# Performance work log

Hardware: AMD Instinct MI355X
Metric: run time of the kernel (lower is better)

## Reference

```python
import jax, jax.numpy as jnp
import numpy as np

B, T, P, D, H = 4, 12, 196, 512, 8
DH = D // H
EPS = 1e-6


def _norm(x, alpha, bias):
    # torch Norm: alpha*(x-mean)/(std_unbiased+eps)+bias, std uses Bessel correction (ddof=1)
    mu = jnp.mean(x, axis=-1, keepdims=True)
    sd = jnp.std(x, axis=-1, ddof=1, keepdims=True)
    return alpha * (x - mu) / (sd + EPS) + bias


def setup_inputs() -> dict:
    key = jax.random.key(0)
    ks = jax.random.split(key, 12)
    s = 0.02

    def n(k, shape, scale=s):
        return jax.random.normal(k, shape, jnp.float32) * scale

    return {
        "x": jax.random.normal(ks[0], (B, T, P, D), jnp.float32),
        "Wq": n(ks[1], (D, D)), "bq": jnp.zeros((D,), jnp.float32),
        "Wk": n(ks[2], (D, D)), "bk": jnp.zeros((D,), jnp.float32),
        "Wv": n(ks[3], (D, D)), "bv": jnp.zeros((D,), jnp.float32),
        "in_a": jnp.ones((D,), jnp.float32), "in_b": jnp.zeros((D,), jnp.float32),
        "attn_a": jnp.ones((D,), jnp.float32), "attn_b": jnp.zeros((D,), jnp.float32),
        "out_a": jnp.ones((D,), jnp.float32), "out_b": jnp.zeros((D,), jnp.float32),
        "Wt": n(ks[4], (T, D, D)), "bt": jnp.zeros((T, D), jnp.float32),
        "pos": n(ks[5], (T, T, P, D), 0.02),
        "W1": n(ks[6], (2 * D, D)), "b1": jnp.zeros((2 * D,), jnp.float32),
        "W2": n(ks[7], (D, 2 * D)), "b2": jnp.zeros((D,), jnp.float32),
    }


def reference(x, Wq, bq, Wk, bk, Wv, bv, in_a, in_b, attn_a, attn_b,
              out_a, out_b, Wt, bt, pos, W1, b1, W2, b2):
    x2 = _norm(x, in_a, in_b)

    def proj(W, b):
        # [B,T,P,D] -> [B,T,H,P,DH]
        return (x2 @ W.T + b).reshape(B, T, P, H, DH).transpose(0, 1, 3, 2, 4)

    Q = proj(Wq, bq)
    K = proj(Wk, bk)
    V = proj(Wv, bv)

    # all-pairs temporal cross attention: [B,t,u,H,Pq,Pk]
    qk = jnp.einsum('btijk,builk->btuijl', Q, K) / np.sqrt(DH)
    attn = jax.nn.softmax(qk, axis=-1)  # no mask, dropout=0
    av = jnp.einsum('btuijl,builk->btuijk', attn, V)  # [B,t,u,H,P,DH]
    av = av.transpose(0, 1, 2, 4, 3, 5).reshape(B, T, T, P, D)
    av = _norm(av, attn_a, attn_b)
    x2p = av + pos  # pos broadcasts over batch

    # per-u Linear fused as one batched contraction, summed over u
    tc = jnp.einsum('btupd,ued->btpe', x2p / T, Wt) + jnp.sum(bt, axis=0)
    x = x + jax.nn.gelu(tc, approximate=False)

    x2 = _norm(x, out_a, out_b)
    h = jax.nn.gelu(x2 @ W1.T + b1, approximate=False)
    y = jax.nn.gelu(h @ W2.T + b2, approximate=False)
    return x + y
```

## Files before the change

kernel.cpp:

```cpp
#include <hip/hip_runtime.h>
#include <hip/hip_bf16.h>

typedef __hip_bfloat16 bf16;

typedef __bf16 bfrag8 __attribute__((ext_vector_type(8)));
typedef __bf16 bfrag4 __attribute__((ext_vector_type(4)));
typedef float  ffrag4 __attribute__((ext_vector_type(4)));
typedef float  ffrag16 __attribute__((ext_vector_type(16)));

#define EPS 1e-6f

__device__ __forceinline__ float gelu_exact(float v) {
  return 0.5f * v * (1.0f + erff(v * 0.7071067811865475f));
}

__device__ __forceinline__ void async16(const void* g, void* s) {
  __builtin_amdgcn_global_load_lds(
      (const __attribute__((address_space(1))) unsigned int*)g,
      (__attribute__((address_space(3))) unsigned int*)s, 16, 0, 0);
}

struct alignas(16) bf16x8 { bf16 v[8]; };
struct alignas(4)  bf16p2 { __bf16 v[2]; };

__global__ __launch_bounds__(256) void zero_acc_kernel(float* __restrict__ p) {
  size_t i = ((size_t)blockIdx.x * 256 + threadIdx.x) * 4;
  *(float4*)(p + i) = make_float4(0.f, 0.f, 0.f, 0.f);
}

__global__ __launch_bounds__(256) void conv_w_kernel(
    const float* __restrict__ Wq, const float* __restrict__ Wk,
    const float* __restrict__ Wv, const float* __restrict__ W1,
    const float* __restrict__ W2, const float* __restrict__ Wt,
    __bf16* __restrict__ dst)
{
  size_t e = ((size_t)blockIdx.x * 256 + threadIdx.x) * 8;
  const float* src; size_t off, dsto;
  if      (e <  262144) { src = Wq; off = e;           dsto = e; }
  else if (e <  524288) { src = Wk; off = e -  262144; dsto = e; }
  else if (e <  786432) { src = Wv; off = e -  524288; dsto = e; }
  else if (e < 1310720) { src = W1; off = e -  786432; dsto = e; }
  else if (e < 1835008) { src = W2; off = e - 1310720; dsto = e; }
  else if (e < 4980736) {
    src = Wt; off = e - 1835008;
    size_t u = off >> 18;
    size_t rem = off & 262143;
    size_t eo = rem >> 9, d = rem & 511;
    dsto = 1835008 + eo * 6144 + u * 512 + d;
  }
  else return;
  float4 f0 = *(const float4*)(src + off);
  float4 f1 = *(const float4*)(src + off + 4);
  bfrag8 o;
  o[0] = (__bf16)f0.x; o[1] = (__bf16)f0.y; o[2] = (__bf16)f0.z; o[3] = (__bf16)f0.w;
  o[4] = (__bf16)f1.x; o[5] = (__bf16)f1.y; o[6] = (__bf16)f1.z; o[7] = (__bf16)f1.w;
  *(bfrag8*)(dst + dsto) = o;
}

__global__ __launch_bounds__(512) void sum_bt_kernel(
    const float* __restrict__ bt, float* __restrict__ sbt)
{
  int n = threadIdx.x;
  float s = 0.f;
#pragma unroll
  for (int u = 0; u < 12; ++u) s += bt[u * 512 + n];
  sbt[n] = s;
}

__global__ __launch_bounds__(64) void norm_f32_to_bf16_kernel(
    const float* __restrict__ in, __bf16* __restrict__ out,
    const float* __restrict__ alpha, const float* __restrict__ beta)
{
  size_t row = blockIdx.x;
  int l = threadIdx.x;
  const float* r = in + row * 512 + l * 8;
  float4 v0 = *(const float4*)(r);
  float4 v1 = *(const float4*)(r + 4);
  float f[8] = {v0.x, v0.y, v0.z, v0.w, v1.x, v1.y, v1.z, v1.w};
  float s = 0.f, ss = 0.f;
#pragma unroll
  for (int q = 0; q < 8; ++q) { s += f[q]; ss += f[q] * f[q]; }
#pragma unroll
  for (int off = 32; off; off >>= 1) { s += __shfl_xor(s, off); ss += __shfl_xor(ss, off); }
  float mu = s * (1.f / 512.f);
  float var = fmaxf((ss - 512.f * mu * mu) * (1.f / 511.f), 0.f);
  float inv = 1.f / (sqrtf(var) + EPS);
  const float* al = alpha + l * 8;
  const float* be = beta + l * 8;
  float4 a0 = *(const float4*)al, a1 = *(const float4*)(al + 4);
  float4 b0 = *(const float4*)be, b1 = *(const float4*)(be + 4);
  float aa[8] = {a0.x, a0.y, a0.z, a0.w, a1.x, a1.y, a1.z, a1.w};
  float bb[8] = {b0.x, b0.y, b0.z, b0.w, b1.x, b1.y, b1.z, b1.w};
  bfrag8 o;
#pragma unroll
  for (int q = 0; q < 8; ++q) o[q] = (__bf16)(aa[q] * (f[q] - mu) * inv + bb[q]);
  *(bfrag8*)(out + row * 512 + l * 8) = o;
}

__global__ __launch_bounds__(256) void norm_av_kernel(
    bf16* __restrict__ av, const float* __restrict__ alpha,
    const float* __restrict__ beta, const float* __restrict__ pos)
{
  size_t row = (size_t)blockIdx.x * 4 + (threadIdx.x >> 6);
  int l = threadIdx.x & 63;
  bf16* r = av + row * 512 + (size_t)l * 8;
  bf16x8 ib = *(const bf16x8*)r;
  float f[8];
#pragma unroll
  for (int q = 0; q < 8; ++q) f[q] = __bfloat162float(ib.v[q]);
  float s = 0.f, ss = 0.f;
#pragma unroll
  for (int q = 0; q < 8; ++q) { s += f[q]; ss += f[q] * f[q]; }
#pragma unroll
  for (int off = 32; off; off >>= 1) { s += __shfl_xor(s, off); ss += __shfl_xor(ss, off); }
  float mu = s * (1.f / 512.f);
  float var = fmaxf((ss - 512.f * mu * mu) * (1.f / 511.f), 0.f);
  float inv = 1.f / (sqrtf(var) + EPS);
  size_t prow = row % 28224;
  const float* pr = pos + prow * 512 + l * 8;
  float4 p0 = *(const float4*)pr, p1 = *(const float4*)(pr + 4);
  const float* al = alpha + l * 8;
  const float* be = beta + l * 8;
  float4 a0 = *(const float4*)al, a1 = *(const float4*)(al + 4);
  float4 b0 = *(const float4*)be, b1 = *(const float4*)(be + 4);
  float pa[8] = {p0.x, p0.y, p0.z, p0.w, p1.x, p1.y, p1.z, p1.w};
  float aa[8] = {a0.x, a0.y, a0.z, a0.w, a1.x, a1.y, a1.z, a1.w};
  float bb[8] = {b0.x, b0.y, b0.z, b0.w, b1.x, b1.y, b1.z, b1.w};
  bf16x8 ob;
#pragma unroll
  for (int q = 0; q < 8; ++q)
    ob.v[q] = __float2bfloat16(aa[q] * (f[q] - mu) * inv + bb[q] + pa[q]);
  *(bf16x8*)r = ob;
}

__global__ __launch_bounds__(256) void mfma_nt_kernel(
    const __bf16* __restrict__ A,
    const __bf16* __restrict__ Bq, const __bf16* __restrict__ Bk,
    const __bf16* __restrict__ Bv,
    const float* __restrict__ bq, const float* __restrict__ bk,
    const float* __restrict__ bv,
    __bf16* __restrict__ oq, __bf16* __restrict__ ok, __bf16* __restrict__ ov,
    const float* __restrict__ res, float* __restrict__ fout,
    int K, int mode)
{
  __shared__ __bf16 As[2 * 128 * 32];
  __shared__ __bf16 Bs[2 * 128 * 32];
  int tid = threadIdx.x;

  int nwg = gridDim.x * gridDim.y;
  int cpx = nwg >> 3;
  int lid = blockIdx.x + gridDim.x * blockIdx.y;
  int logical = (lid & 7) * cpx + (lid >> 3);
  int bx = logical % gridDim.x;
  int by = logical / gridDim.x;
  int m0 = by * 128;
  int n0g = bx * 128;

  const __bf16* Bsel; const float* biassel; __bf16* osel; int ncol0;
  if (mode == 0) {
    int sel = n0g >> 9;
    Bsel = sel == 0 ? Bq : (sel == 1 ? Bk : Bv);
    biassel = sel == 0 ? bq : (sel == 1 ? bk : bv);
    osel = sel == 0 ? oq : (sel == 1 ? ok : ov);
    ncol0 = n0g & 511;
  } else {
    Bsel = Bq; biassel = bq; osel = oq; ncol0 = n0g;
  }

  int srow = tid >> 2;
  int scol = ((tid & 3) ^ ((srow >> 1) & 3)) * 8;
  int rg0 = m0 + srow;       if (rg0 > 9407) rg0 = 9407;
  int rg1 = m0 + 64 + srow;  if (rg1 > 9407) rg1 = 9407;
  const __bf16* a0 = A + (size_t)rg0 * K + scol;
  const __bf16* a1 = A + (size_t)rg1 * K + scol;
  const __bf16* b0 = Bsel + (size_t)(ncol0 + srow) * K + scol;
  const __bf16* b1 = Bsel + (size_t)(ncol0 + 64 + srow) * K + scol;
  char* sa0 = (char*)As + tid * 16;
  char* sa1 = (char*)As + 4096 + tid * 16;
  char* sb0 = (char*)Bs + tid * 16;
  char* sb1 = (char*)Bs + 4096 + tid * 16;

  int l = tid & 63, w = tid >> 6;
  int lm = l & 15, lq = l >> 4;
  int wm = w >> 1, wn = w & 1;
  int rsw = ((((lm >> 1) & 3) ^ lq)) * 8;

  const int nsteps = K >> 5;
  async16(a0, sa0);
  async16(a1, sa1);
  async16(b0, sb0);
  async16(b1, sb1);
  __syncthreads();

  ffrag4 acc[4][4] = {};
  int cur = 0;
  for (int t = 0; t < nsteps; ++t) {
    if (t + 1 < nsteps) {
      int k1 = (t + 1) << 5;
      int bo = (cur ^ 1) * 8192;
      async16(a0 + k1, sa0 + bo);
      async16(a1 + k1, sa1 + bo);
      async16(b0 + k1, sb0 + bo);
      async16(b1 + k1, sb1 + bo);
    }
    int co = cur * 4096;
    bfrag8 af[4], bfr[4];
#pragma unroll
    for (int i = 0; i < 4; ++i)
      af[i] = *(const bfrag8*)&As[co + (wm * 64 + i * 16 + lm) * 32 + rsw];
#pragma unroll
    for (int j = 0; j < 4; ++j)
      bfr[j] = *(const bfrag8*)&Bs[co + (wn * 64 + j * 16 + lm) * 32 + rsw];
#pragma unroll
    for (int i = 0; i < 4; ++i)
#pragma unroll
      for (int j = 0; j < 4; ++j)
        acc[i][j] = __builtin_amdgcn_mfma_f32_16x16x32_bf16(af[i], bfr[j], acc[i][j], 0, 0, 0);
    __syncthreads();
    cur ^= 1;
  }

#pragma unroll
  for (int i = 0; i < 4; ++i) {
    int mbase = m0 + wm * 64 + i * 16 + lq * 4;
#pragma unroll
    for (int j = 0; j < 4; ++j) {
      int n = ncol0 + wn * 64 + j * 16 + lm;
      float bj = biassel[n];
#pragma unroll
      for (int r = 0; r < 4; ++r) {
        int mr = mbase + r;
        if (mr < 9408) {
          float v = acc[i][j][r] + bj;
          if (mode == 0)      osel[(size_t)mr * 512 + n] = (__bf16)v;
          else if (mode == 1) osel[(size_t)mr * 1024 + n] = (__bf16)gelu_exact(v);
          else                fout[(size_t)mr * 512 + n] =
                                res[(size_t)mr * 512 + n] + gelu_exact(v);
        }
      }
    }
  }
}

__global__ __launch_bounds__(256) void mfma_tc_kernel(
    const __bf16* __restrict__ X2p, const __bf16* __restrict__ Wte,
    float* __restrict__ accb)
{
  __shared__ __bf16 As[2 * 128 * 32];
  __shared__ __bf16 Bs[2 * 128 * 32];
  int tid = threadIdx.x;

  int lid = blockIdx.x + 4 * (blockIdx.y + 74 * blockIdx.z);
  int logical = (lid & 7) * 148 + (lid >> 3);
  int lx = logical & 3;
  int rest = logical >> 2;
  int ly = rest % 74;
  int lz = rest / 74;

  int m0 = ly * 128;
  int n0 = lx * 128;
  int kbeg = lz * 1536;

  int srow = tid >> 2;
  int scol = ((tid & 3) ^ ((srow >> 1) & 3)) * 8;
  int rg0 = m0 + srow;       if (rg0 > 9407) rg0 = 9407;
  int rg1 = m0 + 64 + srow;  if (rg1 > 9407) rg1 = 9407;
  int btq0 = rg0 / 196, p0_ = rg0 - btq0 * 196;
  int btq1 = rg1 / 196, p1_ = rg1 - btq1 * 196;
  const __bf16* a0 = X2p + (size_t)btq0 * 1204224 + (size_t)p0_ * 512 + scol;
  const __bf16* a1 = X2p + (size_t)btq1 * 1204224 + (size_t)p1_ * 512 + scol;
  const __bf16* b0 = Wte + (size_t)(n0 + srow) * 6144 + scol;
  const __bf16* b1 = Wte + (size_t)(n0 + 64 + srow) * 6144 + scol;
  char* sa0 = (char*)As + tid * 16;
  char* sa1 = (char*)As + 4096 + tid * 16;
  char* sb0 = (char*)Bs + tid * 16;
  char* sb1 = (char*)Bs + 4096 + tid * 16;

  int l = tid & 63, w = tid >> 6;
  int lm = l & 15, lq = l >> 4;
  int wm = w >> 1, wn = w & 1;
  int rsw = ((((lm >> 1) & 3) ^ lq)) * 8;

  {
    size_t aoff = (size_t)(kbeg >> 9) * 100352 + (size_t)(kbeg & 511);
    async16(a0 + aoff, sa0);
    async16(a1 + aoff, sa1);
    async16(b0 + kbeg, sb0);
    async16(b1 + kbeg, sb1);
  }
  __syncthreads();

  ffrag4 acc[4][4] = {};
  int cur = 0;
  for (int t = 0; t < 48; ++t) {
    if (t + 1 < 48) {
      int k1 = kbeg + (t + 1) * 32;
      size_t aoff = (size_t)(k1 >> 9) * 100352 + (size_t)(k1 & 511);
      int bo = (cur ^ 1) * 8192;
      async16(a0 + aoff, sa0 + bo);
      async16(a1 + aoff, sa1 + bo);
      async16(b0 + k1, sb0 + bo);
      async16(b1 + k1, sb1 + bo);
    }
    int co = cur * 4096;
    bfrag8 af[4], bfr[4];
#pragma unroll
    for (int i = 0; i < 4; ++i)
      af[i] = *(const bfrag8*)&As[co + (wm * 64 + i * 16 + lm) * 32 + rsw];
#pragma unroll
    for (int j = 0; j < 4; ++j)
      bfr[j] = *(const bfrag8*)&Bs[co + (wn * 64 + j * 16 + lm) * 32 + rsw];
#pragma unroll
    for (int i = 0; i < 4; ++i)
#pragma unroll
      for (int j = 0; j < 4; ++j)
        acc[i][j] = __builtin_amdgcn_mfma_f32_16x16x32_bf16(af[i], bfr[j], acc[i][j], 0, 0, 0);
    __syncthreads();
    cur ^= 1;
  }

#pragma unroll
  for (int i = 0; i < 4; ++i) {
    int mbase = m0 + wm * 64 + i * 16 + lq * 4;
#pragma unroll
    for (int j = 0; j < 4; ++j) {
      int n = n0 + wn * 64 + j * 16 + lm;
#pragma unroll
      for (int r = 0; r < 4; ++r) {
        int mr = mbase + r;
        if (mr < 9408)
          atomicAdd(accb + (size_t)mr * 512 + n, acc[i][j][r]);
      }
    }
  }
}

__global__ __launch_bounds__(64) void tc_epi_norm_kernel(
    const float* __restrict__ accb, const float* __restrict__ x,
    const float* __restrict__ sbt,
    const float* __restrict__ alpha, const float* __restrict__ beta,
    float* __restrict__ xmid, __bf16* __restrict__ x3b)
{
  size_t row = blockIdx.x;
  int l = threadIdx.x;
  size_t base = row * 512 + l * 8;
  float4 c0 = *(const float4*)(accb + base);
  float4 c1 = *(const float4*)(accb + base + 4);
  float4 x0 = *(const float4*)(x + base);
  float4 x1 = *(const float4*)(x + base + 4);
  float4 s0 = *(const float4*)(sbt + l * 8);
  float4 s1 = *(const float4*)(sbt + l * 8 + 4);
  float cc[8] = {c0.x, c0.y, c0.z, c0.w, c1.x, c1.y, c1.z, c1.w};
  float xx[8] = {x0.x, x0.y, x0.z, x0.w, x1.x, x1.y, x1.z, x1.w};
  float sv[8] = {s0.x, s0.y, s0.z, s0.w, s1.x, s1.y, s1.z, s1.w};
  float f[8];
#pragma unroll
  for (int q = 0; q < 8; ++q)
    f[q] = xx[q] + gelu_exact(cc[q] * (1.f / 12.f) + sv[q]);
  *(float4*)(xmid + base)     = make_float4(f[0], f[1], f[2], f[3]);
  *(float4*)(xmid + base + 4) = make_float4(f[4], f[5], f[6], f[7]);
  float s = 0.f, ss = 0.f;
#pragma unroll
  for (int q = 0; q < 8; ++q) { s += f[q]; ss += f[q] * f[q]; }
#pragma unroll
  for (int off = 32; off; off >>= 1) { s += __shfl_xor(s, off); ss += __shfl_xor(ss, off); }
  float mu = s * (1.f / 512.f);
  float var = fmaxf((ss - 512.f * mu * mu) * (1.f / 511.f), 0.f);
  float inv = 1.f / (sqrtf(var) + EPS);
  const float* al = alpha + l * 8;
  const float* be = beta + l * 8;
  float4 a0 = *(const float4*)al, a1 = *(const float4*)(al + 4);
  float4 b0 = *(const float4*)be, b1 = *(const float4*)(be + 4);
  float aa[8] = {a0.x, a0.y, a0.z, a0.w, a1.x, a1.y, a1.z, a1.w};
  float bb[8] = {b0.x, b0.y, b0.z, b0.w, b1.x, b1.y, b1.z, b1.w};
  bfrag8 o;
#pragma unroll
  for (int q = 0; q < 8; ++q) o[q] = (__bf16)(aa[q] * (f[q] - mu) * inv + bb[q]);
  *(bfrag8*)(x3b + base) = o;
}

__global__ __launch_bounds__(512, 4) void attn_kernel(
    const __bf16* __restrict__ Q, const __bf16* __restrict__ K,
    const __bf16* __restrict__ V, __bf16* __restrict__ av)
{
  __shared__ __bf16 Ks[196 * 64];
  __shared__ __bf16 Vt[64 * 208];
  __shared__ __bf16 Pball[8 * 32 * 20];

  int bid = blockIdx.x;
  int half = bid & 1;
  int h = (bid >> 1) & 7;
  int r0 = bid >> 4;
  int u = r0 % 12;
  int b = r0 / 12;

  const __bf16* Kp = K + ((size_t)(b * 12 + u) * 196) * 512 + h * 64;
  const __bf16* Vp = V + ((size_t)(b * 12 + u) * 196) * 512 + h * 64;

  for (int idx = threadIdx.x; idx < 196 * 8; idx += 512) {
    int r = idx >> 3, g = idx & 7;
    *(bfrag8*)&Ks[r * 64 + ((g ^ (r & 7)) * 8)] =
        *(const bfrag8*)&Kp[(size_t)r * 512 + g * 8];
  }
  for (int idx = threadIdx.x; idx < 64 * 6; idx += 512) {
    int r = idx / 6, c2 = 196 + (idx % 6) * 2;
    bf16p2 z; z.v[0] = (__bf16)0.f; z.v[1] = (__bf16)0.f;
    *(bf16p2*)&Vt[r * 208 + c2] = z;
  }
  for (int idx = threadIdx.x; idx < 98 * 8; idx += 512) {
    int r2 = (idx % 98) * 2, c8 = (idx / 98) * 8;
    bfrag8 va = *(const bfrag8*)&Vp[(size_t)r2 * 512 + c8];
    bfrag8 vb = *(const bfrag8*)&Vp[(size_t)(r2 + 1) * 512 + c8];
#pragma unroll
    for (int e = 0; e < 8; ++e) {
      bf16p2 pr; pr.v[0] = va[e]; pr.v[1] = vb[e];
      *(bf16p2*)&Vt[(c8 + e) * 208 + r2] = pr;
    }
  }
  __syncthreads();

  int w = threadIdx.x >> 6, l = threadIdx.x & 63;
  int l5 = l >> 5, c = l & 31;
  __bf16* Pb = Pball + w * (32 * 20);

  for (int unit = w; unit < 42; unit += 8) {
    int t = unit / 7, qt = unit - t * 7;
    int tq = half * 6 + t;
    const __bf16* Qp = Q + ((size_t)(b * 12 + tq) * 196) * 512 + h * 64;
    __bf16* avp = av + ((size_t)((b * 12 + tq) * 12 + u) * 196) * 512 + h * 64;
    int q0 = qt * 32;

    const __bf16* qp = Qp + (size_t)(q0 + c) * 512 + l5 * 8;
    bfrag8 qf[4];
    qf[0] = *(const bfrag8*)(qp);
    qf[1] = *(const bfrag8*)(qp + 16);
    qf[2] = *(const bfrag8*)(qp + 32);
    qf[3] = *(const bfrag8*)(qp + 48);

    ffrag16 O0, O1;
#pragma unroll
    for (int g = 0; g < 16; ++g) { O0[g] = 0.f; O1[g] = 0.f; }
    float sumacc = 0.f;

    for (int nt = 0; nt < 7; ++nt) {
      int key = nt * 32 + c; if (key > 195) key = 195;
      const __bf16* kbase = &Ks[key * 64];
      int kx = key & 7;

      ffrag16 s;
#pragma unroll
      for (int g = 0; g < 16; ++g) s[g] = 0.f;
#pragma unroll
      for (int kc = 0; kc < 4; ++kc) {
        bfrag8 kf = *(const bfrag8*)&kbase[(((kc * 2 + l5) ^ kx) * 8)];
        s = __builtin_amdgcn_mfma_f32_32x32x16_bf16(kf, qf[kc], s, 0, 0, 0);
      }

#pragma unroll
      for (int g = 0; g < 16; ++g) {
        float e = __expf(s[g] * 0.125f);
        bool keep = (nt < 6) || ((g < 4) && (l5 == 0));
        e = keep ? e : 0.f;
        s[g] = e;
        sumacc += e;
      }

#pragma unroll
      for (int sub = 0; sub < 2; ++sub) {
        if (nt == 6 && sub == 1) break;
#pragma unroll
        for (int g = 0; g < 8; ++g) {
          int gg = sub * 8 + g;
          int k16 = (gg & 3) + 8 * ((gg >> 2) & 1) + 4 * l5;
          Pb[c * 20 + k16] = (__bf16)s[gg];
        }
        __threadfence_block();
        int ch = nt * 2 + sub;
        bfrag4 plo = *(const bfrag4*)&Pb[c * 20 + l5 * 8];
        bfrag4 phi = *(const bfrag4*)&Pb[c * 20 + l5 * 8 + 4];
        bfrag8 pa = __builtin_shufflevector(plo, phi, 0, 1, 2, 3, 4, 5, 6, 7);
        bfrag8 v0 = *(const bfrag8*)&Vt[(size_t)(c     ) * 208 + ch * 16 + l5 * 8];
        bfrag8 v1 = *(const bfrag8*)&Vt[(size_t)(c + 32) * 208 + ch * 16 + l5 * 8];
        O0 = __builtin_amdgcn_mfma_f32_32x32x16_bf16(pa, v0, O0, 0, 0, 0);
        O1 = __builtin_amdgcn_mfma_f32_32x32x16_bf16(pa, v1, O1, 0, 0, 0);
      }
    }

    float stot = sumacc + __shfl_xor(sumacc, 32);

#pragma unroll
    for (int g = 0; g < 16; ++g) {
      int row = (g & 3) + 8 * (g >> 2) + 4 * l5;
      float sq = __shfl(stot, row);
      float iv = __builtin_amdgcn_rcpf(sq);
      int q = q0 + row;
      if (q < 196) {
        size_t base = (size_t)q * 512 + c;
        avp[base]      = (__bf16)(O0[g] * iv);
        avp[base + 32] = (__bf16)(O1[g] * iv);
      }
    }
  }
}

extern "C" void kernel_launch(void* const* d_in, const int* in_sizes, int n_in,
                              void* d_out, int out_size, void* d_ws, size_t ws_size,
                              hipStream_t stream)
{
  const float* x      = (const float*)d_in[0];
  const float* Wq     = (const float*)d_in[1];
  const float* bq     = (const float*)d_in[2];
  const float* Wk     = (const float*)d_in[3];
  const float* bk     = (const float*)d_in[4];
  const float* Wv     = (const float*)d_in[5];
  const float* bv     = (const float*)d_in[6];
  const float* in_a   = (const float*)d_in[7];
  const float* in_b   = (const float*)d_in[8];
  const float* attn_a = (const float*)d_in[9];
  const float* attn_b = (const float*)d_in[10];
  const float* out_a  = (const float*)d_in[11];
  const float* out_b  = (const float*)d_in[12];
  const float* Wt     = (const float*)d_in[13];
  const float* bt     = (const float*)d_in[14];
  const float* pos    = (const float*)d_in[15];
  const float* W1     = (const float*)d_in[16];
  const float* b1     = (const float*)d_in[17];
  const float* W2     = (const float*)d_in[18];
  const float* b2     = (const float*)d_in[19];

  char* ws = (char*)d_ws;
  const size_t bfb = (size_t)9408 * 512 * 2;
  __bf16* x2b  = (__bf16*)(ws);
  __bf16* Qb   = (__bf16*)(ws + bfb);
  __bf16* Kb   = (__bf16*)(ws + 2 * bfb);
  __bf16* Vb   = (__bf16*)(ws + 3 * bfb);
  __bf16* av   = (__bf16*)(ws + 4 * bfb);
  char*   wreg = ws + 4 * bfb + (size_t)115605504;
  __bf16* Wqb  = (__bf16*)(wreg);
  __bf16* Wkb  = (__bf16*)(wreg) + 262144;
  __bf16* Wvb  = (__bf16*)(wreg) + 524288;
  __bf16* W1b  = (__bf16*)(wreg) + 786432;
  __bf16* W2b  = (__bf16*)(wreg) + 1310720;
  __bf16* Wtb  = (__bf16*)(wreg) + 1835008;
  float*  sbt  = (float*)(wreg + 9961472);
  float*  accb = (float*)(wreg + 9963520);
  float*  xmid = (float*)(ws);
  __bf16* x3b  = (__bf16*)(ws + 2 * bfb);
  __bf16* hb   = (__bf16*)(ws + 4 * bfb);
  float*  out  = (float*)d_out;

  conv_w_kernel<<<2432, 256, 0, stream>>>(Wq, Wk, Wv, W1, W2, Wt, (__bf16*)wreg);
  sum_bt_kernel<<<1, 512, 0, stream>>>(bt, sbt);
  zero_acc_kernel<<<4704, 256, 0, stream>>>(accb);
  norm_f32_to_bf16_kernel<<<9408, 64, 0, stream>>>(x, x2b, in_a, in_b);
  mfma_nt_kernel<<<dim3(12, 74), 256, 0, stream>>>(
      x2b, Wqb, Wkb, Wvb, bq, bk, bv, Qb, Kb, Vb, nullptr, nullptr, 512, 0);
  attn_kernel<<<768, 512, 0, stream>>>(Qb, Kb, Vb, av);
  norm_av_kernel<<<28224, 256, 0, stream>>>((bf16*)av, attn_a, attn_b, pos);
  mfma_tc_kernel<<<dim3(4, 74, 4), 256, 0, stream>>>(av, Wtb, accb);
  tc_epi_norm_kernel<<<9408, 64, 0, stream>>>(accb, x, sbt, out_a, out_b, xmid, x3b);
  mfma_nt_kernel<<<dim3(8, 74), 256, 0, stream>>>(
      x3b, W1b, nullptr, nullptr, b1, nullptr, nullptr, hb, nullptr, nullptr,
      nullptr, nullptr, 512, 1);
  mfma_nt_kernel<<<dim3(4, 74), 256, 0, stream>>>(
      hb, W2b, nullptr, nullptr, b2, nullptr, nullptr, nullptr, nullptr, nullptr,
      xmid, out, 1024, 2);
}
```

Measured before the change: 544.7 us.

## Triple-buffer LDS tiles with two-deep async prefetch in MFMA GEMM kernels

Both MFMA GEMM kernels move from double- to triple-buffered shared memory tiles and prefetch two K-steps ahead. The full __syncthreads is replaced by a partial s_waitcnt vmcnt(4) plus a raw s_barrier, so one stage of global-to-LDS loads can stay in flight across the barrier. The goal is to hide global load latency behind MFMA work. In exchange, LDS per block grows from 32KB to 48KB, which may lower occupancy, and correctness now depends on manual vmcnt accounting matching the compiler's emitted loads.

```diff
diff --git a/kernel.cpp b/kernel.cpp
--- a/kernel.cpp
+++ b/kernel.cpp
@@ -143,8 +143,8 @@
     const float* __restrict__ res, float* __restrict__ fout,
     int K, int mode)
 {
-  __shared__ __bf16 As[2 * 128 * 32];
-  __shared__ __bf16 Bs[2 * 128 * 32];
+  __shared__ __bf16 As[3 * 128 * 32];
+  __shared__ __bf16 Bs[3 * 128 * 32];
   int tid = threadIdx.x;
 
   int nwg = gridDim.x * gridDim.y;
@@ -186,22 +186,24 @@
   int rsw = ((((lm >> 1) & 3) ^ lq)) * 8;
 
   const int nsteps = K >> 5;
-  async16(a0, sa0);
-  async16(a1, sa1);
-  async16(b0, sb0);
-  async16(b1, sb1);
-  __syncthreads();
+  async16(a0, sa0); async16(a1, sa1);
+  async16(b0, sb0); async16(b1, sb1);
+  async16(a0 + 32, sa0 + 8192); async16(a1 + 32, sa1 + 8192);
+  async16(b0 + 32, sb0 + 8192); async16(b1 + 32, sb1 + 8192);
+  __builtin_amdgcn_sched_barrier(0);
+  asm volatile("s_waitcnt vmcnt(4)" ::: "memory");
+  __builtin_amdgcn_s_barrier();
+  __builtin_amdgcn_sched_barrier(0);
 
   ffrag4 acc[4][4] = {};
   int cur = 0;
   for (int t = 0; t < nsteps; ++t) {
-    if (t + 1 < nsteps) {
-      int k1 = (t + 1) << 5;
-      int bo = (cur ^ 1) * 8192;
-      async16(a0 + k1, sa0 + bo);
-      async16(a1 + k1, sa1 + bo);
-      async16(b0 + k1, sb0 + bo);
-      async16(b1 + k1, sb1 + bo);
+    if (t + 2 < nsteps) {
+      int k2 = (t + 2) << 5;
+      int nb = cur + 2; if (nb >= 3) nb -= 3;
+      int bo = nb * 8192;
+      async16(a0 + k2, sa0 + bo); async16(a1 + k2, sa1 + bo);
+      async16(b0 + k2, sb0 + bo); async16(b1 + k2, sb1 + bo);
     }
     int co = cur * 4096;
     bfrag8 af[4], bfr[4];
@@ -216,8 +218,12 @@
 #pragma unroll
       for (int j = 0; j < 4; ++j)
         acc[i][j] = __builtin_amdgcn_mfma_f32_16x16x32_bf16(af[i], bfr[j], acc[i][j], 0, 0, 0);
-    __syncthreads();
-    cur ^= 1;
+    __builtin_amdgcn_sched_barrier(0);
+    if (t + 2 < nsteps) asm volatile("s_waitcnt vmcnt(4)" ::: "memory");
+    else                asm volatile("s_waitcnt vmcnt(0)" ::: "memory");
+    __builtin_amdgcn_s_barrier();
+    __builtin_amdgcn_sched_barrier(0);
+    cur += 1; if (cur == 3) cur = 0;
   }
 
 #pragma unroll
@@ -246,8 +252,8 @@
     const __bf16* __restrict__ X2p, const __bf16* __restrict__ Wte,
     float* __restrict__ accb)
 {
-  __shared__ __bf16 As[2 * 128 * 32];
-  __shared__ __bf16 Bs[2 * 128 * 32];
+  __shared__ __bf16 As[3 * 128 * 32];
+  __shared__ __bf16 Bs[3 * 128 * 32];
   int tid = threadIdx.x;
 
   int lid = blockIdx.x + 4 * (blockIdx.y + 74 * blockIdx.z);
@@ -282,25 +288,29 @@
   int rsw = ((((lm >> 1) & 3) ^ lq)) * 8;
 
   {
-    size_t aoff = (size_t)(kbeg >> 9) * 100352 + (size_t)(kbeg & 511);
-    async16(a0 + aoff, sa0);
-    async16(a1 + aoff, sa1);
-    async16(b0 + kbeg, sb0);
-    async16(b1 + kbeg, sb1);
-  }
-  __syncthreads();
+    size_t ao0 = (size_t)(kbeg >> 9) * 100352 + (size_t)(kbeg & 511);
+    int k1 = kbeg + 32;
+    size_t ao1 = (size_t)(k1 >> 9) * 100352 + (size_t)(k1 & 511);
+    async16(a0 + ao0, sa0); async16(a1 + ao0, sa1);
+    async16(b0 + kbeg, sb0); async16(b1 + kbeg, sb1);
+    async16(a0 + ao1, sa0 + 8192); async16(a1 + ao1, sa1 + 8192);
+    async16(b0 + k1, sb0 + 8192); async16(b1 + k1, sb1 + 8192);
+  }
+  __builtin_amdgcn_sched_barrier(0);
+  asm volatile("s_waitcnt vmcnt(4)" ::: "memory");
+  __builtin_amdgcn_s_barrier();
+  __builtin_amdgcn_sched_barrier(0);
 
   ffrag4 acc[4][4] = {};
   int cur = 0;
   for (int t = 0; t < 48; ++t) {
-    if (t + 1 < 48) {
-      int k1 = kbeg + (t + 1) * 32;
-      size_t aoff = (size_t)(k1 >> 9) * 100352 + (size_t)(k1 & 511);
-      int bo = (cur ^ 1) * 8192;
-      async16(a0 + aoff, sa0 + bo);
-      async16(a1 + aoff, sa1 + bo);
-      async16(b0 + k1, sb0 + bo);
-      async16(b1 + k1, sb1 + bo);
+    if (t + 2 < 48) {
+      int k2 = kbeg + (t + 2) * 32;
+      size_t aoff = (size_t)(k2 >> 9) * 100352 + (size_t)(k2 & 511);
+      int nb = cur + 2; if (nb >= 3) nb -= 3;
+      int bo = nb * 8192;
+      async16(a0 + aoff, sa0 + bo); async16(a1 + aoff, sa1 + bo);
+      async16(b0 + k2, sb0 + bo); async16(b1 + k2, sb1 + bo);
     }
     int co = cur * 4096;
     bfrag8 af[4], bfr[4];
@@ -315,8 +325,12 @@
 #pragma unroll
       for (int j = 0; j < 4; ++j)
         acc[i][j] = __builtin_amdgcn_mfma_f32_16x16x32_bf16(af[i], bfr[j], acc[i][j], 0, 0, 0);
-    __syncthreads();
-    cur ^= 1;
+    __builtin_amdgcn_sched_barrier(0);
+    if (t + 2 < 48) asm volatile("s_waitcnt vmcnt(4)" ::: "memory");
+    else            asm volatile("s_waitcnt vmcnt(0)" ::: "memory");
+    __builtin_amdgcn_s_barrier();
+    __builtin_amdgcn_sched_barrier(0);
+    cur += 1; if (cur == 3) cur = 0;
   }
 
 #pragma unroll
```

Result: no change. 550.8 us (+1.1%).
